# Optimization experiments

Measured on AMD Instinct MI355X. Metric: run time of the kernel, lower is better.

## Reference

```python
import jax, jax.numpy as jnp
import numpy as np

B, S, D, H = 2, 2048, 1024, 16
HD = D // H  # head_size = 64

def setup_inputs() -> dict:
    key = jax.random.key(0)
    ks = jax.random.split(key, 8)
    sc = 0.02
    return {
        "q": jax.random.normal(ks[0], (B, S, D), jnp.float32),
        "k": jax.random.normal(ks[1], (B, S, D), jnp.float32),
        "v": jax.random.normal(ks[2], (B, S, D), jnp.float32),
        "padding_mask": jnp.zeros((B, 1, 1, S), jnp.float32),
        "Wq": jax.random.normal(ks[3], (D, D), jnp.float32) * sc,
        "bq": jnp.zeros((D,), jnp.float32),
        "Wk": jax.random.normal(ks[4], (D, D), jnp.float32) * sc,
        "bk": jnp.zeros((D,), jnp.float32),
        "Wv": jax.random.normal(ks[5], (D, D), jnp.float32) * sc,
        "bv": jnp.zeros((D,), jnp.float32),
        "Wo": jax.random.normal(ks[6], (D, D), jnp.float32) * sc,
        "bo": jnp.zeros((D,), jnp.float32),
    }

def reference(q, k, v, padding_mask, Wq, bq, Wk, bk, Wv, bv, Wo, bo):
    b = q.shape[0]
    qh = (q @ Wq + bq).reshape(b, -1, H, HD)
    kh = (k @ Wk + bk).reshape(b, -1, H, HD)
    vh = (v @ Wv + bv).reshape(b, -1, H, HD)
    # [B, H, Sq, Sk] scores, materialized as in the original
    qk = jnp.einsum('bjhd,bkhd->bhjk', qh, kh) / jnp.sqrt(jnp.float32(HD))
    qk = qk + padding_mask * -1e12
    attn = jax.nn.softmax(qk, axis=-1)
    qkv = jnp.einsum('bhjk,bkhd->bjhd', attn, vh).reshape(b, -1, D)
    return qkv @ Wo + bo
```

## Files before the change

### kernel.cpp

```cpp
#include <hip/hip_runtime.h>
#include <math.h>

typedef __bf16 bf16_t;
typedef __bf16 bf16x8 __attribute__((ext_vector_type(8)));
typedef __bf16 bf16x4v __attribute__((ext_vector_type(4)));
typedef float f32x4 __attribute__((ext_vector_type(4)));
typedef float f32x16 __attribute__((ext_vector_type(16)));

#define LOG2E 1.4426950408889634f
#define MBIAS_C (-1e12f * LOG2E)

#if __has_builtin(__builtin_amdgcn_exp2f)
#define EXP2F(x) __builtin_amdgcn_exp2f(x)
#else
#define EXP2F(x) exp2f(x)
#endif

typedef __attribute__((address_space(1))) const unsigned int g_u32;
typedef __attribute__((address_space(3))) unsigned int l_u32;
__device__ __forceinline__ void load_lds_16B(const void* g, void* l){
  __builtin_amdgcn_global_load_lds((g_u32*)g, (l_u32*)l, 16, 0, 0);
}

__device__ __forceinline__ f32x16 zero16(){
  f32x16 z;
  #pragma unroll
  for (int i = 0; i < 16; i++) z[i] = 0.f;
  return z;
}

typedef union { bf16x4v b4; uint2 u2; } pk8;
typedef union { uint2 h[2]; bf16x8 b8; } pk16;

__global__ __launch_bounds__(256) void cast3_kernel(const float* __restrict__ q,
                                                    const float* __restrict__ k,
                                                    const float* __restrict__ v,
                                                    bf16_t* __restrict__ out){
  int z = blockIdx.y;
  const float* x = (z == 0) ? q : (z == 1) ? k : v;
  int i = blockIdx.x * 256 + threadIdx.x;
  float4 f = reinterpret_cast<const float4*>(x)[i];
  bf16x4v w;
  w[0] = (bf16_t)f.x; w[1] = (bf16_t)f.y; w[2] = (bf16_t)f.z; w[3] = (bf16_t)f.w;
  reinterpret_cast<bf16x4v*>(out + (size_t)z * 4194304)[i] = w;
}

__global__ __launch_bounds__(256) void wtrans4_kernel(const float* __restrict__ Wq,
                                                      const float* __restrict__ Wk,
                                                      const float* __restrict__ Wv,
                                                      const float* __restrict__ Wo,
                                                      bf16_t* __restrict__ Wcat,
                                                      bf16_t* __restrict__ Wot){
  __shared__ float T[32][33];
  int z = blockIdx.z;
  const float* W = (z == 0) ? Wq : (z == 1) ? Wk : (z == 2) ? Wv : Wo;
  bf16_t* dst = (z < 3) ? (Wcat + (size_t)z * 1024 * 1024) : Wot;
  int x = threadIdx.x, y = threadIdx.y;
  int k0 = blockIdx.y * 32, n0 = blockIdx.x * 32;
  #pragma unroll
  for (int i = 0; i < 4; i++) T[y + 8*i][x] = W[(size_t)(k0 + y + 8*i) * 1024 + n0 + x];
  __syncthreads();
  #pragma unroll
  for (int i = 0; i < 4; i++) dst[(size_t)(n0 + y + 8*i) * 1024 + k0 + x] = (bf16_t)T[x][y + 8*i];
}

__device__ __forceinline__ void qkv_epilogue(f32x4 (&acc)[4][4], int seg, int n0g, int m0,
                                             int wm, int wn, int l16, int lq,
                                             const float* bias, bf16_t* qp, bf16_t* kp,
                                             bf16_t* vh){
  bf16_t* Cp = (seg == 0) ? qp : (seg == 1) ? kp : vh;
  float scale = (seg == 0) ? 0.125f * LOG2E : 1.0f;
  #pragma unroll
  for (int ti = 0; ti < 4; ti++){
    #pragma unroll
    for (int tj = 0; tj < 4; tj++){
      int col = (n0g + wn + tj*16 + l16) & 1023;
      float bvv = bias[col];
      #pragma unroll
      for (int r = 0; r < 4; r++){
        int row = m0 + wm + ti*16 + lq*4 + r;
        Cp[(size_t)row * 1024 + col] = (bf16_t)((acc[ti][tj][r] + bvv) * scale);
      }
    }
  }
}

__global__ __launch_bounds__(256) void gemm_qkv_bf(const bf16_t* __restrict__ qkvin,
                                                   const bf16_t* __restrict__ Wcat,
                                                   const float* __restrict__ bq,
                                                   const float* __restrict__ bk,
                                                   const float* __restrict__ bv,
                                                   bf16_t* __restrict__ qp,
                                                   bf16_t* __restrict__ kp,
                                                   bf16_t* __restrict__ vh){
  const int K = 1024;
  __shared__ __align__(16) bf16_t As[128*32];
  __shared__ __align__(16) bf16_t Bs[128*32];
  int tid = threadIdx.x, wave = tid >> 6, lane = tid & 63;
  int l16 = lane & 15, lq = lane >> 4;
  int n0g = blockIdx.x * 128;
  int seg = n0g >> 10;
  const bf16_t* A   = qkvin + (size_t)seg * 4194304;
  const float* bias = (seg == 0) ? bq : (seg == 1) ? bk : bv;
  int m0 = blockIdx.y * 128;
  int wm = (wave >> 1) * 64, wn = (wave & 1) * 64;
  int cposR = lq ^ ((l16 >> 2) & 3);
  f32x4 acc[4][4] = {};
  for (int kt = 0; kt < K; kt += 32){
    __syncthreads();
    #pragma unroll
    for (int i = 0; i < 2; i++){
      int u = tid + 256*i;
      int r = u >> 2, cpos = u & 3, cg = cpos ^ ((r >> 2) & 3);
      int ldsoff = (wave*64 + 256*i) * 16;
      load_lds_16B(&A[(size_t)(m0 + r) * K + kt + cg*8], (char*)As + ldsoff);
      load_lds_16B(&Wcat[(size_t)(n0g + r) * K + kt + cg*8], (char*)Bs + ldsoff);
    }
    __syncthreads();
    bf16x8 af[4], bfr[4];
    #pragma unroll
    for (int t = 0; t < 4; t++) af[t]  = *reinterpret_cast<bf16x8*>(&As[(wm + t*16 + l16)*32 + cposR*8]);
    #pragma unroll
    for (int t = 0; t < 4; t++) bfr[t] = *reinterpret_cast<bf16x8*>(&Bs[(wn + t*16 + l16)*32 + cposR*8]);
    #pragma unroll
    for (int ti = 0; ti < 4; ti++)
      #pragma unroll
      for (int tj = 0; tj < 4; tj++)
        acc[ti][tj] = __builtin_amdgcn_mfma_f32_16x16x32_bf16(af[ti], bfr[tj], acc[ti][tj], 0, 0, 0);
  }
  qkv_epilogue(acc, seg, n0g, m0, wm, wn, l16, lq, bias, qp, kp, vh);
}

__global__ __launch_bounds__(256) void gemm_qkv_f32(const float* __restrict__ qi,
                                                    const float* __restrict__ ki,
                                                    const float* __restrict__ vi,
                                                    const bf16_t* __restrict__ Wcat,
                                                    const float* __restrict__ bq,
                                                    const float* __restrict__ bk,
                                                    const float* __restrict__ bv,
                                                    bf16_t* __restrict__ qp,
                                                    bf16_t* __restrict__ kp,
                                                    bf16_t* __restrict__ vh){
  const int K = 1024;
  __shared__ __align__(16) float  Asf[128*32];
  __shared__ __align__(16) bf16_t Bs[128*32];
  int tid = threadIdx.x, wave = tid >> 6, lane = tid & 63;
  int l16 = lane & 15, lq = lane >> 4;
  int n0g = blockIdx.x * 128;
  int seg = n0g >> 10;
  const float* A    = (seg == 0) ? qi : (seg == 1) ? ki : vi;
  const float* bias = (seg == 0) ? bq : (seg == 1) ? bk : bv;
  int m0 = blockIdx.y * 128;
  int wm = (wave >> 1) * 64, wn = (wave & 1) * 64;
  int cposR = lq ^ ((l16 >> 2) & 3);
  int ca0 = (2*lq)     ^ (l16 & 7);
  int ca1 = (2*lq + 1) ^ (l16 & 7);
  f32x4 acc[4][4] = {};
  for (int kt = 0; kt < K; kt += 32){
    __syncthreads();
    #pragma unroll
    for (int i = 0; i < 4; i++){
      int u = tid + 256*i;
      int r = u >> 3, cpos = u & 7, cg = cpos ^ (r & 7);
      load_lds_16B(&A[(size_t)(m0 + r) * K + kt + cg*4], (char*)Asf + (wave*64 + 256*i)*16);
    }
    #pragma unroll
    for (int i = 0; i < 2; i++){
      int u = tid + 256*i;
      int r = u >> 2, cpos = u & 3, cg = cpos ^ ((r >> 2) & 3);
      load_lds_16B(&Wcat[(size_t)(n0g + r) * K + kt + cg*8], (char*)Bs + (wave*64 + 256*i)*16);
    }
    __syncthreads();
    bf16x8 af[4], bfr[4];
    #pragma unroll
    for (int t = 0; t < 4; t++){
      int row = wm + t*16 + l16;
      f32x4 x0 = *reinterpret_cast<f32x4*>(&Asf[row*32 + ca0*4]);
      f32x4 x1 = *reinterpret_cast<f32x4*>(&Asf[row*32 + ca1*4]);
      bf16x8 a;
      a[0] = (bf16_t)x0[0]; a[1] = (bf16_t)x0[1]; a[2] = (bf16_t)x0[2]; a[3] = (bf16_t)x0[3];
      a[4] = (bf16_t)x1[0]; a[5] = (bf16_t)x1[1]; a[6] = (bf16_t)x1[2]; a[7] = (bf16_t)x1[3];
      af[t] = a;
    }
    #pragma unroll
    for (int t = 0; t < 4; t++) bfr[t] = *reinterpret_cast<bf16x8*>(&Bs[(wn + t*16 + l16)*32 + cposR*8]);
    #pragma unroll
    for (int ti = 0; ti < 4; ti++)
      #pragma unroll
      for (int tj = 0; tj < 4; tj++)
        acc[ti][tj] = __builtin_amdgcn_mfma_f32_16x16x32_bf16(af[ti], bfr[tj], acc[ti][tj], 0, 0, 0);
  }
  qkv_epilogue(acc, seg, n0g, m0, wm, wn, l16, lq, bias, qp, kp, vh);
}

__global__ __launch_bounds__(256) void gemm_out(const bf16_t* __restrict__ A,
                                                const bf16_t* __restrict__ Bt,
                                                const float* __restrict__ bias,
                                                float* __restrict__ C){
  const int K = 1024, N = 1024;
  __shared__ __align__(16) bf16_t As[128*64];
  __shared__ __align__(16) bf16_t Bs[64*64];
  int tid = threadIdx.x, wave = tid >> 6, lane = tid & 63;
  int l16 = lane & 15, lq = lane >> 4;
  int m0 = blockIdx.y * 128, n0 = blockIdx.x * 64;
  int wm = wave * 32;
  f32x4 acc[2][4] = {};
  for (int kt = 0; kt < K; kt += 64){
    __syncthreads();
    #pragma unroll
    for (int i = 0; i < 4; i++){
      int u = tid + 256*i;
      int r = u >> 3, cpos = u & 7, cg = cpos ^ (r & 7);
      load_lds_16B(&A[(size_t)(m0 + r) * K + kt + cg*8], (char*)As + (wave*64 + 256*i)*16);
    }
    #pragma unroll
    for (int i = 0; i < 2; i++){
      int u = tid + 256*i;
      int r = u >> 3, cpos = u & 7, cg = cpos ^ (r & 7);
      load_lds_16B(&Bt[(size_t)(n0 + r) * K + kt + cg*8], (char*)Bs + (wave*64 + 256*i)*16);
    }
    __syncthreads();
    #pragma unroll
    for (int kk = 0; kk < 2; kk++){
      bf16x8 af[2], bfr[4];
      #pragma unroll
      for (int t = 0; t < 2; t++){
        int row = wm + t*16 + l16, cpos = (kk*4 + lq) ^ (l16 & 7);
        af[t] = *reinterpret_cast<bf16x8*>(&As[row*64 + cpos*8]);
      }
      #pragma unroll
      for (int t = 0; t < 4; t++){
        int row = t*16 + l16, cpos = (kk*4 + lq) ^ (l16 & 7);
        bfr[t] = *reinterpret_cast<bf16x8*>(&Bs[row*64 + cpos*8]);
      }
      #pragma unroll
      for (int ti = 0; ti < 2; ti++)
        #pragma unroll
        for (int tj = 0; tj < 4; tj++)
          acc[ti][tj] = __builtin_amdgcn_mfma_f32_16x16x32_bf16(af[ti], bfr[tj], acc[ti][tj], 0, 0, 0);
    }
  }
  #pragma unroll
  for (int ti = 0; ti < 2; ti++){
    #pragma unroll
    for (int tj = 0; tj < 4; tj++){
      int col = n0 + tj*16 + l16;
      float bvv = bias[col];
      #pragma unroll
      for (int r = 0; r < 4; r++){
        int row = m0 + wm + ti*16 + lq*4 + r;
        C[(size_t)row * N + col] = acc[ti][tj][r] + bvv;
      }
    }
  }
}

__global__ __launch_bounds__(256) void vtrans_kernel(const bf16_t* __restrict__ vh,
                                                     bf16_t* __restrict__ Vt){
  __shared__ bf16_t T[64][72];
  int tid = threadIdx.x;
  int s0 = blockIdx.x * 64, h = blockIdx.y, b = blockIdx.z;
  #pragma unroll
  for (int i = 0; i < 2; i++){
    int u = tid + 256*i;
    int r = u >> 3, c = (u & 7) * 8;
    *reinterpret_cast<uint4*>(&T[r][c]) =
      *reinterpret_cast<const uint4*>(&vh[(size_t)(b*2048 + s0 + r) * 1024 + h*64 + c]);
  }
  __syncthreads();
  #pragma unroll
  for (int i = 0; i < 2; i++){
    int u = tid + 256*i;
    int d = u >> 3, cs = (u & 7) * 8;
    bf16_t t8[8];
    #pragma unroll
    for (int j = 0; j < 8; j++) t8[j] = T[cs + j][d];
    *reinterpret_cast<uint4*>(&Vt[(size_t)((b*16 + h)*64 + d) * 2048 + s0 + cs]) =
      *reinterpret_cast<uint4*>(t8);
  }
}

__global__ __launch_bounds__(256) void attn_kernel(const bf16_t* __restrict__ qp,
                                                   const bf16_t* __restrict__ kp,
                                                   const bf16_t* __restrict__ vt,
                                                   const float* __restrict__ mask,
                                                   bf16_t* __restrict__ ctx){
  const int S = 2048, D = 1024, HD = 64;
  __shared__ __align__(16) char smem[25216];
  bf16_t* Ks   = (bf16_t*)smem;
  bf16_t* Vts  = (bf16_t*)(smem + 8192);
  float*  Mb   = (float*)(smem + 16384);
  float*  Lsum = (float*)(smem + 24576);
  float*  Lcomb= (float*)(smem + 24832);
  float*  Opart= (float*)smem;
  int tid = threadIdx.x, wave = tid >> 6, lane = tid & 63;
  int l32 = lane & 31, H = lane >> 5;
  int qhalf = wave & 1, khalf = wave >> 1;
  int qt = blockIdx.x, h = blockIdx.y, b = blockIdx.z;
  const bf16_t* Qg = qp + (size_t)b*S*D + h*HD;
  const bf16_t* Kg = kp + (size_t)b*S*D + h*HD;
  const bf16_t* Vg = vt + (size_t)(b*16 + h)*HD*S;
  const float*  Mg = mask + (size_t)b*S;

  #pragma unroll
  for (int i = 0; i < 2; i++)
    load_lds_16B(&Mg[(tid + 256*i)*4], (char*)Mb + (wave*64 + 256*i)*16);

  int qrow = qt*64 + qhalf*32 + l32;
  bf16x8 qf[4];
  #pragma unroll
  for (int s = 0; s < 4; s++)
    qf[s] = *reinterpret_cast<const bf16x8*>(&Qg[(size_t)qrow * D + s*16 + 8*H]);

  f32x16 o0 = zero16(), o1 = zero16();
  float lacc = 0.f;
  int krow = khalf*32 + l32;

  for (int kt = 0; kt < S; kt += 64){
    __syncthreads();
    #pragma unroll
    for (int i = 0; i < 2; i++){
      int u = tid + 256*i;
      int r = u >> 3, c = u & 7, cg = c ^ (r & 7);
      load_lds_16B(&Kg[(size_t)(kt + r) * D + cg*8], (char*)Ks + (wave*64 + 256*i)*16);
    }
    #pragma unroll
    for (int i = 0; i < 2; i++){
      int u = tid + 256*i;
      int r = u >> 3, c = u & 7, cg = c ^ (r & 7);
      load_lds_16B(&Vg[(size_t)r * S + kt + cg*8], (char*)Vts + (wave*64 + 256*i)*16);
    }
    __syncthreads();

    f32x16 sc;
    #pragma unroll
    for (int s = 0; s < 4; s++){
      int cp = (2*s + H) ^ (l32 & 7);
      bf16x8 kf = *reinterpret_cast<bf16x8*>(&Ks[krow*64 + cp*8]);
      if (s == 0) sc = __builtin_amdgcn_mfma_f32_32x32x16_bf16(kf, qf[0], zero16(), 0, 0, 0);
      else        sc = __builtin_amdgcn_mfma_f32_32x32x16_bf16(kf, qf[s], sc, 0, 0, 0);
    }
    pk8 grp[4];
    #pragma unroll
    for (int g = 0; g < 4; g++){
      float4 mv = *reinterpret_cast<float4*>(&Mb[kt + khalf*32 + 8*g + 4*H]);
      float p0 = EXP2F(fmaf(mv.x, MBIAS_C, sc[4*g+0]));
      float p1 = EXP2F(fmaf(mv.y, MBIAS_C, sc[4*g+1]));
      float p2 = EXP2F(fmaf(mv.z, MBIAS_C, sc[4*g+2]));
      float p3 = EXP2F(fmaf(mv.w, MBIAS_C, sc[4*g+3]));
      lacc += (p0 + p1) + (p2 + p3);
      pk8 w;
      w.b4[0] = (bf16_t)p0; w.b4[1] = (bf16_t)p1; w.b4[2] = (bf16_t)p2; w.b4[3] = (bf16_t)p3;
      grp[g] = w;
    }
    #pragma unroll
    for (int kk = 0; kk < 2; kk++){
      uint2 ga = grp[2*kk].u2;
      uint2 gb = grp[2*kk+1].u2;
      uint2 send = H ? ga : gb;
      uint2 recv;
      recv.x = (unsigned)__shfl_xor((int)send.x, 32);
      recv.y = (unsigned)__shfl_xor((int)send.y, 32);
      pk16 fr;
      fr.h[0] = H ? recv : ga;
      fr.h[1] = H ? gb : recv;
      int cp = (4*khalf + 2*kk + H) ^ (l32 & 7);
      bf16x8 vf0 = *reinterpret_cast<bf16x8*>(&Vts[l32*64 + cp*8]);
      bf16x8 vf1 = *reinterpret_cast<bf16x8*>(&Vts[(32 + l32)*64 + cp*8]);
      o0 = __builtin_amdgcn_mfma_f32_32x32x16_bf16(fr.b8, vf0, o0, 0, 0, 0);
      o1 = __builtin_amdgcn_mfma_f32_32x32x16_bf16(fr.b8, vf1, o1, 0, 0, 0);
    }
  }
  float lfull = lacc + __shfl_xor(lacc, 32);
  __syncthreads();
  if (khalf == 1){
    #pragma unroll
    for (int reg = 0; reg < 16; reg++){
      Opart[qhalf*2048 + reg*64 + lane]        = o0[reg];
      Opart[qhalf*2048 + 1024 + reg*64 + lane] = o1[reg];
    }
    if (H == 0) Lsum[qhalf*32 + l32] = lfull;
  }
  __syncthreads();
  if (khalf == 0){
    #pragma unroll
    for (int reg = 0; reg < 16; reg++){
      o0[reg] += Opart[qhalf*2048 + reg*64 + lane];
      o1[reg] += Opart[qhalf*2048 + 1024 + reg*64 + lane];
    }
    lfull += Lsum[qhalf*32 + l32];
    Lcomb[qhalf*32 + l32] = lfull;
    #pragma unroll
    for (int g = 0; g < 4; g++){
      f32x4 lv = *reinterpret_cast<f32x4*>(&Lcomb[qhalf*32 + 8*g + 4*H]);
      #pragma unroll
      for (int r = 0; r < 4; r++){
        float inv = 1.f / lv[r];
        int grow = qt*64 + qhalf*32 + 8*g + 4*H + r;
        size_t base = (size_t)(b*S + grow) * D + h*HD;
        ctx[base + l32]      = (bf16_t)(o0[4*g + r] * inv);
        ctx[base + 32 + l32] = (bf16_t)(o1[4*g + r] * inv);
      }
    }
  }
}

extern "C" void kernel_launch(void* const* d_in, const int* in_sizes, int n_in,
                              void* d_out, int out_size, void* d_ws, size_t ws_size,
                              hipStream_t stream){
  const float* q    = (const float*)d_in[0];
  const float* k    = (const float*)d_in[1];
  const float* v    = (const float*)d_in[2];
  const float* mask = (const float*)d_in[3];
  const float* Wq   = (const float*)d_in[4];
  const float* bq   = (const float*)d_in[5];
  const float* Wk   = (const float*)d_in[6];
  const float* bk   = (const float*)d_in[7];
  const float* Wv   = (const float*)d_in[8];
  const float* bv   = (const float*)d_in[9];
  const float* Wo   = (const float*)d_in[10];
  const float* bo   = (const float*)d_in[11];

  char* ws = (char*)d_ws;
  bf16_t* qp    = (bf16_t*)(ws);
  bf16_t* kp    = (bf16_t*)(ws + 8388608);
  bf16_t* vh    = (bf16_t*)(ws + 16777216);
  bf16_t* Wcat  = (bf16_t*)(ws + 25165824);
  bf16_t* Wot   = (bf16_t*)(ws + 31457280);
  bf16_t* Vt    = (bf16_t*)(ws + 33554432);
  bf16_t* ctx   = (bf16_t*)(ws + 41943040);
  bf16_t* qkvin = (bf16_t*)(ws + 33554432);

  wtrans4_kernel<<<dim3(32,32,4), dim3(32,8), 0, stream>>>(Wq, Wk, Wv, Wo, Wcat, Wot);
  if (ws_size >= 58720256){
    cast3_kernel<<<dim3(4096,3), 256, 0, stream>>>(q, k, v, qkvin);
    gemm_qkv_bf<<<dim3(24,32), 256, 0, stream>>>(qkvin, Wcat, bq, bk, bv, qp, kp, vh);
  } else {
    gemm_qkv_f32<<<dim3(24,32), 256, 0, stream>>>(q, k, v, Wcat, bq, bk, bv, qp, kp, vh);
  }
  vtrans_kernel<<<dim3(32,16,2), 256, 0, stream>>>(vh, Vt);
  attn_kernel<<<dim3(32,16,2), 256, 0, stream>>>(qp, kp, Vt, mask, ctx);
  gemm_out<<<dim3(16,32), 256, 0, stream>>>(ctx, Wot, bo, (float*)d_out);
}
```

Before: 245.0 us.

## Double-buffer K/V tiles and fold mask bias and row sums into MFMA

The attention kernel now double-buffers K and V tiles in LDS. The next tile is prefetched while the current one is computed, which leaves one barrier per iteration instead of two. A small pre-kernel scales the padding mask by the bias constant, and that result is loaded straight into the QK MFMA accumulator init, removing the per-element FMA. Softmax row sums are computed by an extra MFMA against a ones vector instead of scalar adds. This adds an extra launch and a third MFMA per step, and it reuses the vh workspace region for the scaled mask after vtrans has consumed it.

```diff
diff --git a/kernel.cpp b/kernel.cpp
--- a/kernel.cpp
+++ b/kernel.cpp
@@ -31,6 +31,7 @@
 
 typedef union { bf16x4v b4; uint2 u2; } pk8;
 typedef union { uint2 h[2]; bf16x8 b8; } pk16;
+typedef union { float4 f4[4]; f32x16 v; } cinit_t;
 
 __global__ __launch_bounds__(256) void cast3_kernel(const float* __restrict__ q,
                                                     const float* __restrict__ k,
@@ -43,6 +44,12 @@
   bf16x4v w;
   w[0] = (bf16_t)f.x; w[1] = (bf16_t)f.y; w[2] = (bf16_t)f.z; w[3] = (bf16_t)f.w;
   reinterpret_cast<bf16x4v*>(out + (size_t)z * 4194304)[i] = w;
+}
+
+__global__ __launch_bounds__(256) void mask_scale_kernel(const float* __restrict__ mask,
+                                                         float* __restrict__ ms){
+  int i = blockIdx.x * 256 + threadIdx.x;
+  ms[i] = mask[i] * MBIAS_C;
 }
 
 __global__ __launch_bounds__(256) void wtrans4_kernel(const float* __restrict__ Wq,
@@ -280,19 +287,15 @@
   }
 }
 
-__global__ __launch_bounds__(256) void attn_kernel(const bf16_t* __restrict__ qp,
-                                                   const bf16_t* __restrict__ kp,
-                                                   const bf16_t* __restrict__ vt,
-                                                   const float* __restrict__ mask,
-                                                   bf16_t* __restrict__ ctx){
+__global__ __launch_bounds__(256, 4) void attn_kernel(const bf16_t* __restrict__ qp,
+                                                      const bf16_t* __restrict__ kp,
+                                                      const bf16_t* __restrict__ vt,
+                                                      const float* __restrict__ ms,
+                                                      bf16_t* __restrict__ ctx){
   const int S = 2048, D = 1024, HD = 64;
-  __shared__ __align__(16) char smem[25216];
-  bf16_t* Ks   = (bf16_t*)smem;
-  bf16_t* Vts  = (bf16_t*)(smem + 8192);
-  float*  Mb   = (float*)(smem + 16384);
-  float*  Lsum = (float*)(smem + 24576);
-  float*  Lcomb= (float*)(smem + 24832);
-  float*  Opart= (float*)smem;
+  __shared__ __align__(16) char smem[33024];
+  float* Lsum  = (float*)(smem + 32768);
+  float* Opart = (float*)smem;
   int tid = threadIdx.x, wave = tid >> 6, lane = tid & 63;
   int l32 = lane & 31, H = lane >> 5;
   int qhalf = wave & 1, khalf = wave >> 1;
@@ -300,11 +303,20 @@
   const bf16_t* Qg = qp + (size_t)b*S*D + h*HD;
   const bf16_t* Kg = kp + (size_t)b*S*D + h*HD;
   const bf16_t* Vg = vt + (size_t)(b*16 + h)*HD*S;
-  const float*  Mg = mask + (size_t)b*S;
-
-  #pragma unroll
-  for (int i = 0; i < 2; i++)
-    load_lds_16B(&Mg[(tid + 256*i)*4], (char*)Mb + (wave*64 + 256*i)*16);
+  const float*  Mg = ms + (size_t)b*S;
+
+  auto stage = [&](int kt, int bsel){
+    char* Kd = smem + bsel*8192;
+    char* Vd = smem + 16384 + bsel*8192;
+    #pragma unroll
+    for (int i = 0; i < 2; i++){
+      int u = tid + 256*i;
+      int r = u >> 3, c = u & 7, cg = c ^ (r & 7);
+      int ldsoff = (wave*64 + 256*i) * 16;
+      load_lds_16B(&Kg[(size_t)(kt + r) * D + cg*8], Kd + ldsoff);
+      load_lds_16B(&Vg[(size_t)r * S + kt + cg*8], Vd + ldsoff);
+    }
+  };
 
   int qrow = qt*64 + qhalf*32 + l32;
   bf16x8 qf[4];
@@ -312,43 +324,43 @@
   for (int s = 0; s < 4; s++)
     qf[s] = *reinterpret_cast<const bf16x8*>(&Qg[(size_t)qrow * D + s*16 + 8*H]);
 
-  f32x16 o0 = zero16(), o1 = zero16();
-  float lacc = 0.f;
+  f32x16 o0 = zero16(), o1 = zero16(), lmm = zero16();
   int krow = khalf*32 + l32;
 
+  pk16 ones;
+  ones.h[0].x = 0x3F803F80u; ones.h[0].y = 0x3F803F80u;
+  ones.h[1].x = 0x3F803F80u; ones.h[1].y = 0x3F803F80u;
+
+  stage(0, 0);
+  __syncthreads();
+  int cur = 0;
+
   for (int kt = 0; kt < S; kt += 64){
-    __syncthreads();
-    #pragma unroll
-    for (int i = 0; i < 2; i++){
-      int u = tid + 256*i;
-      int r = u >> 3, c = u & 7, cg = c ^ (r & 7);
-      load_lds_16B(&Kg[(size_t)(kt + r) * D + cg*8], (char*)Ks + (wave*64 + 256*i)*16);
-    }
-    #pragma unroll
-    for (int i = 0; i < 2; i++){
-      int u = tid + 256*i;
-      int r = u >> 3, c = u & 7, cg = c ^ (r & 7);
-      load_lds_16B(&Vg[(size_t)r * S + kt + cg*8], (char*)Vts + (wave*64 + 256*i)*16);
-    }
-    __syncthreads();
+    cinit_t ci;
+    #pragma unroll
+    for (int g = 0; g < 4; g++)
+      ci.f4[g] = *reinterpret_cast<const float4*>(&Mg[kt + khalf*32 + 8*g + 4*H]);
+
+    if (kt + 64 < S) stage(kt + 64, cur ^ 1);
+
+    bf16_t* Ks  = (bf16_t*)(smem + cur*8192);
+    bf16_t* Vts = (bf16_t*)(smem + 16384 + cur*8192);
 
     f32x16 sc;
     #pragma unroll
     for (int s = 0; s < 4; s++){
       int cp = (2*s + H) ^ (l32 & 7);
       bf16x8 kf = *reinterpret_cast<bf16x8*>(&Ks[krow*64 + cp*8]);
-      if (s == 0) sc = __builtin_amdgcn_mfma_f32_32x32x16_bf16(kf, qf[0], zero16(), 0, 0, 0);
+      if (s == 0) sc = __builtin_amdgcn_mfma_f32_32x32x16_bf16(kf, qf[0], ci.v, 0, 0, 0);
       else        sc = __builtin_amdgcn_mfma_f32_32x32x16_bf16(kf, qf[s], sc, 0, 0, 0);
     }
     pk8 grp[4];
     #pragma unroll
     for (int g = 0; g < 4; g++){
-      float4 mv = *reinterpret_cast<float4*>(&Mb[kt + khalf*32 + 8*g + 4*H]);
-      float p0 = EXP2F(fmaf(mv.x, MBIAS_C, sc[4*g+0]));
-      float p1 = EXP2F(fmaf(mv.y, MBIAS_C, sc[4*g+1]));
-      float p2 = EXP2F(fmaf(mv.z, MBIAS_C, sc[4*g+2]));
-      float p3 = EXP2F(fmaf(mv.w, MBIAS_C, sc[4*g+3]));
-      lacc += (p0 + p1) + (p2 + p3);
+      float p0 = EXP2F(sc[4*g+0]);
+      float p1 = EXP2F(sc[4*g+1]);
+      float p2 = EXP2F(sc[4*g+2]);
+      float p3 = EXP2F(sc[4*g+3]);
       pk8 w;
       w.b4[0] = (bf16_t)p0; w.b4[1] = (bf16_t)p1; w.b4[2] = (bf16_t)p2; w.b4[3] = (bf16_t)p3;
       grp[g] = w;
@@ -367,19 +379,25 @@
       int cp = (4*khalf + 2*kk + H) ^ (l32 & 7);
       bf16x8 vf0 = *reinterpret_cast<bf16x8*>(&Vts[l32*64 + cp*8]);
       bf16x8 vf1 = *reinterpret_cast<bf16x8*>(&Vts[(32 + l32)*64 + cp*8]);
-      o0 = __builtin_amdgcn_mfma_f32_32x32x16_bf16(fr.b8, vf0, o0, 0, 0, 0);
-      o1 = __builtin_amdgcn_mfma_f32_32x32x16_bf16(fr.b8, vf1, o1, 0, 0, 0);
-    }
-  }
-  float lfull = lacc + __shfl_xor(lacc, 32);
-  __syncthreads();
+      o0  = __builtin_amdgcn_mfma_f32_32x32x16_bf16(fr.b8, vf0, o0, 0, 0, 0);
+      o1  = __builtin_amdgcn_mfma_f32_32x32x16_bf16(fr.b8, vf1, o1, 0, 0, 0);
+      lmm = __builtin_amdgcn_mfma_f32_32x32x16_bf16(fr.b8, ones.b8, lmm, 0, 0, 0);
+    }
+    __syncthreads();
+    cur ^= 1;
+  }
+
   if (khalf == 1){
     #pragma unroll
     for (int reg = 0; reg < 16; reg++){
       Opart[qhalf*2048 + reg*64 + lane]        = o0[reg];
       Opart[qhalf*2048 + 1024 + reg*64 + lane] = o1[reg];
     }
-    if (H == 0) Lsum[qhalf*32 + l32] = lfull;
+    if (l32 == 0){
+      #pragma unroll
+      for (int reg = 0; reg < 16; reg++)
+        Lsum[qhalf*32 + (reg & 3) + 8*(reg >> 2) + 4*H] = lmm[reg];
+    }
   }
   __syncthreads();
   if (khalf == 0){
@@ -388,14 +406,12 @@
       o0[reg] += Opart[qhalf*2048 + reg*64 + lane];
       o1[reg] += Opart[qhalf*2048 + 1024 + reg*64 + lane];
     }
-    lfull += Lsum[qhalf*32 + l32];
-    Lcomb[qhalf*32 + l32] = lfull;
     #pragma unroll
     for (int g = 0; g < 4; g++){
-      f32x4 lv = *reinterpret_cast<f32x4*>(&Lcomb[qhalf*32 + 8*g + 4*H]);
       #pragma unroll
       for (int r = 0; r < 4; r++){
-        float inv = 1.f / lv[r];
+        float lf = lmm[4*g + r] + Lsum[qhalf*32 + 8*g + 4*H + r];
+        float inv = 1.f / lf;
         int grow = qt*64 + qhalf*32 + 8*g + 4*H + r;
         size_t base = (size_t)(b*S + grow) * D + h*HD;
         ctx[base + l32]      = (bf16_t)(o0[4*g + r] * inv);
@@ -430,6 +446,7 @@
   bf16_t* Vt    = (bf16_t*)(ws + 33554432);
   bf16_t* ctx   = (bf16_t*)(ws + 41943040);
   bf16_t* qkvin = (bf16_t*)(ws + 33554432);
+  float*  msbuf = (float*)(ws + 16777216);
 
   wtrans4_kernel<<<dim3(32,32,4), dim3(32,8), 0, stream>>>(Wq, Wk, Wv, Wo, Wcat, Wot);
   if (ws_size >= 58720256){
@@ -439,6 +456,7 @@
     gemm_qkv_f32<<<dim3(24,32), 256, 0, stream>>>(q, k, v, Wcat, bq, bk, bv, qp, kp, vh);
   }
   vtrans_kernel<<<dim3(32,16,2), 256, 0, stream>>>(vh, Vt);
-  attn_kernel<<<dim3(32,16,2), 256, 0, stream>>>(qp, kp, Vt, mask, ctx);
+  mask_scale_kernel<<<dim3(16), 256, 0, stream>>>(mask, msbuf);
+  attn_kernel<<<dim3(32,16,2), 256, 0, stream>>>(qp, kp, Vt, msbuf, ctx);
   gemm_out<<<dim3(16,32), 256, 0, stream>>>(ctx, Wot, bo, (float*)d_out);
 }
```

New measurement: 239.3 us. 2.3% less time.
